# Optimization experiments

Hardware: AMD Instinct MI355X
Metric: run time of the kernel (lower is better)

The kernel has to match this reference:

```python
import jax, jax.numpy as jnp
import numpy as np

HEAD_NUM = 16

def setup_inputs() -> dict:
    key = jax.random.key(0)
    k1, k2, k3, k4, k5 = jax.random.split(key, 5)
    B, S, F = 4, 2048, 1024
    return {
        "X": jax.random.normal(k1, (B, S, F), dtype=jnp.float32),
        "residual_score": jax.random.normal(k2, (B, S, F), dtype=jnp.float32),
        "wq": jax.random.normal(k3, (F, F), dtype=jnp.float32) * 0.05,
        "wk": jax.random.normal(k4, (F, F), dtype=jnp.float32) * 0.05,
        "wv": jax.random.normal(k5, (F, F), dtype=jnp.float32) * 0.05,
    }

def reference(X, residual_score, wq, wk, wv):
    B, S, F = X.shape
    H = HEAD_NUM
    D = F // H  # head dim
    # Original scales logits by sqrt(seq_len / head_num), not sqrt(head_dim).
    scale = jnp.sqrt(jnp.asarray(S / H, dtype=X.dtype))
    # QKV projections: [B,S,F] @ [F,F] -> [B,S,F], then split features into heads -> [B,H,S,D]
    def proj(w):
        y = jnp.einsum('bsf,fg->bsg', X, w)
        return y.reshape(B, S, H, D).transpose(0, 2, 1, 3)
    q, k, v = proj(wq), proj(wk), proj(wv)
    logits = jnp.einsum('bhsd,bhtd->bhst', q, k) / scale  # [B,H,S,S]
    attn = jax.nn.softmax(logits, axis=-1)
    effect = jnp.einsum('bhst,bhtd->bhsd', attn, v)  # [B,H,S,D]
    all_effects = effect.transpose(0, 2, 1, 3).reshape(B, S, F)
    out = all_effects + residual_score
    return (out, out)
```

## Files before the change

kernel.cpp:

```cpp
#include <hip/hip_runtime.h>
#include <hip/hip_bf16.h>
#include <stdint.h>

#define B_ 4
#define S_ 2048
#define F_ 1024
#define H_ 16
#define D_ 64
#define M_ (B_*S_)
#define OUTHALF ((size_t)B_*S_*F_)
#define KVB 64
#define QBLK 128

typedef __attribute__((ext_vector_type(4))) float f32x4;
typedef __attribute__((ext_vector_type(8))) short bf16x8;

__device__ __forceinline__ short f2bf(float f) {
  __hip_bfloat16 h = __float2bfloat16(f);
  return *reinterpret_cast<short*>(&h);
}

__device__ __forceinline__ void gl2lds16(const short* g, short* l) {
  __builtin_amdgcn_global_load_lds(
      (const __attribute__((address_space(1))) uint32_t*)g,
      (__attribute__((address_space(3))) uint32_t*)l, 16, 0, 0);
}

__global__ __launch_bounds__(256) void convert_x(const float* __restrict__ X,
                                                 short* __restrict__ Xb) {
  int i = (blockIdx.x * 256 + threadIdx.x) * 8;
  f32x4 a = *(const f32x4*)(X + i);
  f32x4 b = *(const f32x4*)(X + i + 4);
  bf16x8 o;
  o[0]=f2bf(a[0]); o[1]=f2bf(a[1]); o[2]=f2bf(a[2]); o[3]=f2bf(a[3]);
  o[4]=f2bf(b[0]); o[5]=f2bf(b[1]); o[6]=f2bf(b[2]); o[7]=f2bf(b[3]);
  *(bf16x8*)(Xb + i) = o;
}

__global__ __launch_bounds__(256) void transpose_w(
    const float* __restrict__ wq, const float* __restrict__ wk, const float* __restrict__ wv,
    short* __restrict__ tq, short* __restrict__ tk, short* __restrict__ tv) {
  const float* W = blockIdx.z == 0 ? wq : (blockIdx.z == 1 ? wk : wv);
  short* T = blockIdx.z == 0 ? tq : (blockIdx.z == 1 ? tk : tv);
  __shared__ float tile[32][33];
  int tx = threadIdx.x, ty = threadIdx.y;
  int x = blockIdx.x * 32 + tx;
  int y0 = blockIdx.y * 32;
  #pragma unroll
  for (int j = ty; j < 32; j += 8) tile[j][tx] = W[(size_t)(y0 + j) * F_ + x];
  __syncthreads();
  int x2 = y0 + tx;
  int y2 = blockIdx.x * 32;
  #pragma unroll
  for (int j = ty; j < 32; j += 8) T[(size_t)(y2 + j) * F_ + x2] = f2bf(tile[tx][j]);
}

__global__ __launch_bounds__(256) void gemm_qkv(
    const short* __restrict__ Xb,
    const short* __restrict__ Wtq, const short* __restrict__ Wtk, const short* __restrict__ Wtv,
    short* __restrict__ Qb, short* __restrict__ Kb, short* __restrict__ Vt) {
  __shared__ short As[128 * 32];
  __shared__ short Bs[128 * 32];
  const int z = blockIdx.z;
  const short* Wt = z == 0 ? Wtq : (z == 1 ? Wtk : Wtv);
  const int m0 = blockIdx.x * 128, n0 = blockIdx.y * 128;
  const int tid = threadIdx.x, wid = tid >> 6, lane = tid & 63;
  const int wm = wid >> 1, wn = wid & 1;
  const int l15 = lane & 15, l4 = lane >> 4;

  f32x4 acc[4][4];
  #pragma unroll
  for (int i = 0; i < 4; ++i)
    #pragma unroll
    for (int j = 0; j < 4; ++j) acc[i][j] = {0.f, 0.f, 0.f, 0.f};

  const int srow = wid * 32 + (lane >> 2);
  const int scol = (lane & 3) * 8;

  for (int k0 = 0; k0 < F_; k0 += 32) {
    gl2lds16(Xb + (size_t)(m0 + srow) * F_ + k0 + scol,      &As[(wid * 32) * 32]);
    gl2lds16(Xb + (size_t)(m0 + srow + 16) * F_ + k0 + scol, &As[(wid * 32 + 16) * 32]);
    gl2lds16(Wt + (size_t)(n0 + srow) * F_ + k0 + scol,      &Bs[(wid * 32) * 32]);
    gl2lds16(Wt + (size_t)(n0 + srow + 16) * F_ + k0 + scol, &Bs[(wid * 32 + 16) * 32]);
    __syncthreads();
    bf16x8 a[4], b[4];
    #pragma unroll
    for (int mf = 0; mf < 4; ++mf)
      a[mf] = *(const bf16x8*)&As[(wm * 64 + mf * 16 + l15) * 32 + l4 * 8];
    #pragma unroll
    for (int nf = 0; nf < 4; ++nf)
      b[nf] = *(const bf16x8*)&Bs[(wn * 64 + nf * 16 + l15) * 32 + l4 * 8];
    #pragma unroll
    for (int mf = 0; mf < 4; ++mf)
      #pragma unroll
      for (int nf = 0; nf < 4; ++nf)
        acc[mf][nf] = __builtin_amdgcn_mfma_f32_16x16x32_bf16(a[mf], b[nf], acc[mf][nf], 0, 0, 0);
    __syncthreads();
  }

  const float qscale = 0.12751784477559752f;
  #pragma unroll
  for (int mf = 0; mf < 4; ++mf)
    #pragma unroll
    for (int nf = 0; nf < 4; ++nf)
      #pragma unroll
      for (int r = 0; r < 4; ++r) {
        float v = acc[mf][nf][r];
        int row = m0 + wm * 64 + mf * 16 + l4 * 4 + r;
        int col = n0 + wn * 64 + nf * 16 + l15;
        int bb = row >> 11, s = row & 2047, h = col >> 6, d = col & 63;
        if (z == 0)
          Qb[((size_t)(bb * H_ + h) * S_ + s) * D_ + d] = f2bf(v * qscale);
        else if (z == 1)
          Kb[((size_t)(bb * H_ + h) * S_ + s) * D_ + d] = f2bf(v);
        else {
          int s5 = s & 31;
          int sp = (s & ~31) | (((s5 >> 2) & 3) << 3) | (((s5 >> 4) & 1) << 2) | (s5 & 3);
          Vt[((size_t)(bb * H_ + h) * D_ + d) * S_ + sp] = f2bf(v);
        }
      }
}

__global__ __launch_bounds__(256, 4) void attn_kernel(
    const short* __restrict__ Qb, const short* __restrict__ Kb, const short* __restrict__ Vt,
    const float* __restrict__ resid, float* __restrict__ out) {
  __shared__ short Ks[2][KVB][64];
  __shared__ short Vs[2][D_][KVB];
  const int bh = blockIdx.y;
  const int b = bh >> 4, h = bh & 15;
  const int qbase = blockIdx.x * QBLK;
  const int wid = threadIdx.x >> 6, lane = threadIdx.x & 63;
  const int l15 = lane & 15, l4 = lane >> 4;
  const short* Qp = Qb + (size_t)bh * S_ * D_;
  const short* Kp = Kb + (size_t)bh * S_ * D_;
  const short* Vp = Vt + (size_t)bh * D_ * S_;

  bf16x8 bq[2][2];
  #pragma unroll
  for (int g = 0; g < 2; ++g) {
    int qr = qbase + wid * 32 + g * 16 + l15;
    bq[g][0] = *(const bf16x8*)&Qp[qr * D_ + l4 * 8];
    bq[g][1] = *(const bf16x8*)&Qp[qr * D_ + 32 + l4 * 8];
  }

  bf16x8 aOnes;
  {
    short onebf = (short)0x3F80;
    #pragma unroll
    for (int i = 0; i < 8; ++i) aOnes[i] = (l15 == 0) ? onebf : (short)0;
  }

  const int sr0 = wid * 16 + (lane >> 3);
  const int sr1 = sr0 + 8;
  const int sc0 = ((lane & 7) ^ (sr0 & 7)) * 8;
  const int sc1 = ((lane & 7) ^ (sr1 & 7)) * 8;

  f32x4 acc[2][4];
  f32x4 accl[2];
  #pragma unroll
  for (int g = 0; g < 2; ++g) {
    accl[g] = {0.f, 0.f, 0.f, 0.f};
    #pragma unroll
    for (int df = 0; df < 4; ++df) acc[g][df] = {0.f, 0.f, 0.f, 0.f};
  }

  gl2lds16(Kp + (0 + sr0) * D_ + sc0, &Ks[0][wid * 16][0]);
  gl2lds16(Kp + (0 + sr1) * D_ + sc1, &Ks[0][wid * 16 + 8][0]);
  gl2lds16(Vp + (size_t)sr0 * S_ + 0 + sc0, &Vs[0][wid * 16][0]);
  gl2lds16(Vp + (size_t)sr1 * S_ + 0 + sc1, &Vs[0][wid * 16 + 8][0]);

  const int NT = S_ / KVB;
  for (int t = 0; t < NT; ++t) {
    const int buf = t & 1;
    __syncthreads();
    if (t + 1 < NT) {
      const int kv1 = (t + 1) * KVB;
      gl2lds16(Kp + (kv1 + sr0) * D_ + sc0, &Ks[buf ^ 1][wid * 16][0]);
      gl2lds16(Kp + (kv1 + sr1) * D_ + sc1, &Ks[buf ^ 1][wid * 16 + 8][0]);
      gl2lds16(Vp + (size_t)sr0 * S_ + kv1 + sc0, &Vs[buf ^ 1][wid * 16][0]);
      gl2lds16(Vp + (size_t)sr1 * S_ + kv1 + sc1, &Vs[buf ^ 1][wid * 16 + 8][0]);
    }

    f32x4 sf[2][4];
    #pragma unroll
    for (int g = 0; g < 2; ++g)
      #pragma unroll
      for (int nf = 0; nf < 4; ++nf) sf[g][nf] = {0.f, 0.f, 0.f, 0.f};
    __builtin_amdgcn_s_setprio(1);
    #pragma unroll
    for (int nf = 0; nf < 4; ++nf) {
      int row = nf * 16 + l15;
      int c0 = (l4 ^ (row & 7)) * 8;
      int c1 = ((4 + l4) ^ (row & 7)) * 8;
      bf16x8 ak0 = *(const bf16x8*)&Ks[buf][row][c0];
      bf16x8 ak1 = *(const bf16x8*)&Ks[buf][row][c1];
      #pragma unroll
      for (int g = 0; g < 2; ++g) {
        sf[g][nf] = __builtin_amdgcn_mfma_f32_16x16x32_bf16(ak0, bq[g][0], sf[g][nf], 0, 0, 0);
        sf[g][nf] = __builtin_amdgcn_mfma_f32_16x16x32_bf16(ak1, bq[g][1], sf[g][nf], 0, 0, 0);
      }
    }
    __builtin_amdgcn_s_setprio(0);

    bf16x8 pb[2][2];
    #pragma unroll
    for (int g = 0; g < 2; ++g)
      #pragma unroll
      for (int bb = 0; bb < 2; ++bb) {
        bf16x8 p;
        #pragma unroll
        for (int r = 0; r < 4; ++r) {
          p[r]     = f2bf(__builtin_amdgcn_exp2f(sf[g][2 * bb][r]));
          p[4 + r] = f2bf(__builtin_amdgcn_exp2f(sf[g][2 * bb + 1][r]));
        }
        pb[g][bb] = p;
      }

    __builtin_amdgcn_s_setprio(1);
    #pragma unroll
    for (int bb = 0; bb < 2; ++bb) {
      #pragma unroll
      for (int df = 0; df < 4; ++df) {
        int row = df * 16 + l15;
        bf16x8 av = *(const bf16x8*)&Vs[buf][row][((4 * bb + l4) ^ (row & 7)) * 8];
        acc[0][df] = __builtin_amdgcn_mfma_f32_16x16x32_bf16(av, pb[0][bb], acc[0][df], 0, 0, 0);
        acc[1][df] = __builtin_amdgcn_mfma_f32_16x16x32_bf16(av, pb[1][bb], acc[1][df], 0, 0, 0);
      }
      accl[0] = __builtin_amdgcn_mfma_f32_16x16x32_bf16(aOnes, pb[0][bb], accl[0], 0, 0, 0);
      accl[1] = __builtin_amdgcn_mfma_f32_16x16x32_bf16(aOnes, pb[1][bb], accl[1], 0, 0, 0);
    }
    __builtin_amdgcn_s_setprio(0);
  }

  #pragma unroll
  for (int g = 0; g < 2; ++g) {
    float lg = __shfl(accl[g][0], l15);
    float rl = 1.f / lg;
    int s = qbase + wid * 32 + g * 16 + l15;
    #pragma unroll
    for (int df = 0; df < 4; ++df) {
      size_t oi = ((size_t)b * S_ + s) * F_ + h * D_ + df * 16 + l4 * 4;
      f32x4 rv = *(const f32x4*)&resid[oi];
      f32x4 ov;
      #pragma unroll
      for (int r = 0; r < 4; ++r) ov[r] = acc[g][df][r] * rl + rv[r];
      *(f32x4*)&out[oi] = ov;
      *(f32x4*)&out[oi + OUTHALF] = ov;
    }
  }
}

extern "C" void kernel_launch(void* const* d_in, const int* in_sizes, int n_in,
                              void* d_out, int out_size, void* d_ws, size_t ws_size,
                              hipStream_t stream) {
  (void)in_sizes; (void)n_in; (void)out_size; (void)ws_size;
  const float* X     = (const float*)d_in[0];
  const float* resid = (const float*)d_in[1];
  const float* wq    = (const float*)d_in[2];
  const float* wk    = (const float*)d_in[3];
  const float* wv    = (const float*)d_in[4];
  float* out = (float*)d_out;
  char* ws = (char*)d_ws;
  short* Xb  = (short*)(ws);
  short* Wtq = (short*)(ws + (16u << 20));
  short* Wtk = (short*)(ws + (18u << 20));
  short* Wtv = (short*)(ws + (20u << 20));
  short* Qb  = (short*)(ws + (22u << 20));
  short* Kb  = (short*)(ws + (38u << 20));
  short* Vt  = (short*)(ws + (54u << 20));

  convert_x<<<dim3((M_ * F_) / (256 * 8)), 256, 0, stream>>>(X, Xb);
  transpose_w<<<dim3(32, 32, 3), dim3(32, 8), 0, stream>>>(wq, wk, wv, Wtq, Wtk, Wtv);
  gemm_qkv<<<dim3(M_ / 128, F_ / 128, 3), 256, 0, stream>>>(Xb, Wtq, Wtk, Wtv, Qb, Kb, Vt);
  attn_kernel<<<dim3(S_ / QBLK, B_ * H_), 256, 0, stream>>>(Qb, Kb, Vt, resid, out);
}
```

Baseline: 177.1 us.

## Enlarge QKV GEMM tiles with double-buffered swizzled LDS, widen attention blocks

```diff
diff --git a/kernel.cpp b/kernel.cpp
--- a/kernel.cpp
+++ b/kernel.cpp
@@ -10,7 +10,7 @@
 #define M_ (B_*S_)
 #define OUTHALF ((size_t)B_*S_*F_)
 #define KVB 64
-#define QBLK 128
+#define QBLK 256
 
 typedef __attribute__((ext_vector_type(4))) float f32x4;
 typedef __attribute__((ext_vector_type(8))) short bf16x8;
@@ -25,6 +25,13 @@
       (const __attribute__((address_space(1))) uint32_t*)g,
       (__attribute__((address_space(3))) uint32_t*)l, 16, 0, 0);
 }
+
+#define VMCNT_BAR(N)                                            \
+  do {                                                          \
+    asm volatile("s_waitcnt vmcnt(" #N ")" ::: "memory");       \
+    __builtin_amdgcn_s_barrier();                               \
+    asm volatile("" ::: "memory");                              \
+  } while (0)
 
 __global__ __launch_bounds__(256) void convert_x(const float* __restrict__ X,
                                                  short* __restrict__ Xb) {
@@ -55,58 +62,83 @@
   for (int j = ty; j < 32; j += 8) T[(size_t)(y2 + j) * F_ + x2] = f2bf(tile[tx][j]);
 }
 
-__global__ __launch_bounds__(256) void gemm_qkv(
+__global__ __launch_bounds__(512, 2) void gemm_qkv(
     const short* __restrict__ Xb,
     const short* __restrict__ Wtq, const short* __restrict__ Wtk, const short* __restrict__ Wtv,
     short* __restrict__ Qb, short* __restrict__ Kb, short* __restrict__ Vt) {
-  __shared__ short As[128 * 32];
-  __shared__ short Bs[128 * 32];
+  __shared__ short As[2][256][64];
+  __shared__ short Bs[2][256][64];
   const int z = blockIdx.z;
   const short* Wt = z == 0 ? Wtq : (z == 1 ? Wtk : Wtv);
-  const int m0 = blockIdx.x * 128, n0 = blockIdx.y * 128;
+  const int m0 = blockIdx.x * 256, n0 = blockIdx.y * 256;
   const int tid = threadIdx.x, wid = tid >> 6, lane = tid & 63;
-  const int wm = wid >> 1, wn = wid & 1;
+  const int wm = wid >> 2, wn = wid & 3;
   const int l15 = lane & 15, l4 = lane >> 4;
-
-  f32x4 acc[4][4];
-  #pragma unroll
-  for (int i = 0; i < 4; ++i)
+  const int strow = lane >> 3;
+  const int ssrc = ((lane & 7) ^ strow) * 8;
+
+  f32x4 acc[8][4];
+  #pragma unroll
+  for (int i = 0; i < 8; ++i)
     #pragma unroll
     for (int j = 0; j < 4; ++j) acc[i][j] = {0.f, 0.f, 0.f, 0.f};
 
-  const int srow = wid * 32 + (lane >> 2);
-  const int scol = (lane & 3) * 8;
-
-  for (int k0 = 0; k0 < F_; k0 += 32) {
-    gl2lds16(Xb + (size_t)(m0 + srow) * F_ + k0 + scol,      &As[(wid * 32) * 32]);
-    gl2lds16(Xb + (size_t)(m0 + srow + 16) * F_ + k0 + scol, &As[(wid * 32 + 16) * 32]);
-    gl2lds16(Wt + (size_t)(n0 + srow) * F_ + k0 + scol,      &Bs[(wid * 32) * 32]);
-    gl2lds16(Wt + (size_t)(n0 + srow + 16) * F_ + k0 + scol, &Bs[(wid * 32 + 16) * 32]);
-    __syncthreads();
-    bf16x8 a[4], b[4];
-    #pragma unroll
-    for (int mf = 0; mf < 4; ++mf)
-      a[mf] = *(const bf16x8*)&As[(wm * 64 + mf * 16 + l15) * 32 + l4 * 8];
-    #pragma unroll
-    for (int nf = 0; nf < 4; ++nf)
-      b[nf] = *(const bf16x8*)&Bs[(wn * 64 + nf * 16 + l15) * 32 + l4 * 8];
-    #pragma unroll
-    for (int mf = 0; mf < 4; ++mf)
-      #pragma unroll
-      for (int nf = 0; nf < 4; ++nf)
-        acc[mf][nf] = __builtin_amdgcn_mfma_f32_16x16x32_bf16(a[mf], b[nf], acc[mf][nf], 0, 0, 0);
-    __syncthreads();
+  auto stage = [&](int buf, int k0) {
+    #pragma unroll
+    for (int i = 0; i < 4; ++i) {
+      int rbase = i * 64 + wid * 8;
+      gl2lds16(Xb + (size_t)(m0 + rbase + strow) * F_ + k0 + ssrc, &As[buf][rbase][0]);
+    }
+    #pragma unroll
+    for (int i = 0; i < 4; ++i) {
+      int rbase = i * 64 + wid * 8;
+      gl2lds16(Wt + (size_t)(n0 + rbase + strow) * F_ + k0 + ssrc, &Bs[buf][rbase][0]);
+    }
+  };
+
+  stage(0, 0);
+  const int NT = F_ / 64;
+  for (int t = 0; t < NT; ++t) {
+    const int buf = t & 1;
+    if (t + 1 < NT) {
+      stage(buf ^ 1, (t + 1) * 64);
+      VMCNT_BAR(8);
+    } else {
+      VMCNT_BAR(0);
+    }
+    #pragma unroll
+    for (int ks = 0; ks < 2; ++ks) {
+      bf16x8 a[8], b[4];
+      #pragma unroll
+      for (int mf = 0; mf < 8; ++mf) {
+        int row = wm * 128 + mf * 16 + l15;
+        a[mf] = *(const bf16x8*)&As[buf][row][(((ks * 4 + l4) ^ (row & 7)) * 8)];
+      }
+      #pragma unroll
+      for (int nf = 0; nf < 4; ++nf) {
+        int row = wn * 64 + nf * 16 + l15;
+        b[nf] = *(const bf16x8*)&Bs[buf][row][(((ks * 4 + l4) ^ (row & 7)) * 8)];
+      }
+      __builtin_amdgcn_s_setprio(1);
+      #pragma unroll
+      for (int mf = 0; mf < 8; ++mf)
+        #pragma unroll
+        for (int nf = 0; nf < 4; ++nf)
+          acc[mf][nf] = __builtin_amdgcn_mfma_f32_16x16x32_bf16(a[mf], b[nf], acc[mf][nf], 0, 0, 0);
+      __builtin_amdgcn_s_setprio(0);
+    }
+    __builtin_amdgcn_s_barrier();
   }
 
   const float qscale = 0.12751784477559752f;
   #pragma unroll
-  for (int mf = 0; mf < 4; ++mf)
+  for (int mf = 0; mf < 8; ++mf)
     #pragma unroll
     for (int nf = 0; nf < 4; ++nf)
       #pragma unroll
       for (int r = 0; r < 4; ++r) {
         float v = acc[mf][nf][r];
-        int row = m0 + wm * 64 + mf * 16 + l4 * 4 + r;
+        int row = m0 + wm * 128 + mf * 16 + l4 * 4 + r;
         int col = n0 + wn * 64 + nf * 16 + l15;
         int bb = row >> 11, s = row & 2047, h = col >> 6, d = col & 63;
         if (z == 0)
@@ -121,7 +153,7 @@
       }
 }
 
-__global__ __launch_bounds__(256, 4) void attn_kernel(
+__global__ __launch_bounds__(512, 4) void attn_kernel(
     const short* __restrict__ Qb, const short* __restrict__ Kb, const short* __restrict__ Vt,
     const float* __restrict__ resid, float* __restrict__ out) {
   __shared__ short Ks[2][KVB][64];
@@ -150,10 +182,8 @@
     for (int i = 0; i < 8; ++i) aOnes[i] = (l15 == 0) ? onebf : (short)0;
   }
 
-  const int sr0 = wid * 16 + (lane >> 3);
-  const int sr1 = sr0 + 8;
-  const int sc0 = ((lane & 7) ^ (sr0 & 7)) * 8;
-  const int sc1 = ((lane & 7) ^ (sr1 & 7)) * 8;
+  const int sr = wid * 8 + (lane >> 3);
+  const int ssrc = ((lane & 7) ^ (lane >> 3)) * 8;
 
   f32x4 acc[2][4];
   f32x4 accl[2];
@@ -164,10 +194,8 @@
     for (int df = 0; df < 4; ++df) acc[g][df] = {0.f, 0.f, 0.f, 0.f};
   }
 
-  gl2lds16(Kp + (0 + sr0) * D_ + sc0, &Ks[0][wid * 16][0]);
-  gl2lds16(Kp + (0 + sr1) * D_ + sc1, &Ks[0][wid * 16 + 8][0]);
-  gl2lds16(Vp + (size_t)sr0 * S_ + 0 + sc0, &Vs[0][wid * 16][0]);
-  gl2lds16(Vp + (size_t)sr1 * S_ + 0 + sc1, &Vs[0][wid * 16 + 8][0]);
+  gl2lds16(Kp + (0 + sr) * D_ + ssrc, &Ks[0][wid * 8][0]);
+  gl2lds16(Vp + (size_t)sr * S_ + 0 + ssrc, &Vs[0][wid * 8][0]);
 
   const int NT = S_ / KVB;
   for (int t = 0; t < NT; ++t) {
@@ -175,10 +203,8 @@
     __syncthreads();
     if (t + 1 < NT) {
       const int kv1 = (t + 1) * KVB;
-      gl2lds16(Kp + (kv1 + sr0) * D_ + sc0, &Ks[buf ^ 1][wid * 16][0]);
-      gl2lds16(Kp + (kv1 + sr1) * D_ + sc1, &Ks[buf ^ 1][wid * 16 + 8][0]);
-      gl2lds16(Vp + (size_t)sr0 * S_ + kv1 + sc0, &Vs[buf ^ 1][wid * 16][0]);
-      gl2lds16(Vp + (size_t)sr1 * S_ + kv1 + sc1, &Vs[buf ^ 1][wid * 16 + 8][0]);
+      gl2lds16(Kp + (kv1 + sr) * D_ + ssrc, &Ks[buf ^ 1][wid * 8][0]);
+      gl2lds16(Vp + (size_t)sr * S_ + kv1 + ssrc, &Vs[buf ^ 1][wid * 8][0]);
     }
 
     f32x4 sf[2][4];
@@ -271,6 +297,6 @@
 
   convert_x<<<dim3((M_ * F_) / (256 * 8)), 256, 0, stream>>>(X, Xb);
   transpose_w<<<dim3(32, 32, 3), dim3(32, 8), 0, stream>>>(wq, wk, wv, Wtq, Wtk, Wtv);
-  gemm_qkv<<<dim3(M_ / 128, F_ / 128, 3), 256, 0, stream>>>(Xb, Wtq, Wtk, Wtv, Qb, Kb, Vt);
-  attn_kernel<<<dim3(S_ / QBLK, B_ * H_), 256, 0, stream>>>(Qb, Kb, Vt, resid, out);
-}
+  gemm_qkv<<<dim3(M_ / 256, F_ / 256, 3), 512, 0, stream>>>(Xb, Wtq, Wtk, Wtv, Qb, Kb, Vt);
+  attn_kernel<<<dim3(S_ / QBLK, B_ * H_), 512, 0, stream>>>(Qb, Kb, Vt, resid, out);
+}
```

Result: slower. 192.8 us (+8.9%).
